# Kernel optimization log

Measured on AMD Instinct MI355X. Metric: run time of the kernel, lower is better.

The kernel has to match this reference:

```python
import jax, jax.numpy as jnp
import numpy as np

B, S, E, P, K, H = 32, 512, 1024, 256, 3, 8
KERNELS = 4  # conv repeated KERNELS times then averaged -> identical to a single conv


def setup_inputs() -> dict:
    key = jax.random.key(0)
    ks = jax.random.split(key, 8)
    sc = 0.02
    x = jax.random.normal(ks[0], (B, S, E), jnp.float32)
    # lengths must satisfy 3 <= l <= S-1 so slice [1:l+1] and conv length l-2 are valid
    seq_length = jax.random.randint(ks[1], (B,), 16, S - 1)
    proj_w = jax.random.normal(ks[2], (E, P), jnp.float32) * sc
    proj_b = jnp.zeros((P,), jnp.float32)
    conv_w = jax.random.normal(ks[3], (P, P, K), jnp.float32) * sc  # (out, in, width)
    conv_b = jnp.zeros((P,), jnp.float32)
    attn_w = jax.random.normal(ks[4], (P, H * S), jnp.float32) * sc
    attn_b = jnp.zeros((H * S,), jnp.float32)
    c1_w = jax.random.normal(ks[5], (P, P // 2), jnp.float32) * sc
    c1_b = jnp.zeros((P // 2,), jnp.float32)
    c2_w = jax.random.normal(ks[6], (P // 2, 2), jnp.float32) * sc
    c2_b = jnp.zeros((2,), jnp.float32)
    return dict(x=x, seq_length=seq_length, proj_w=proj_w, proj_b=proj_b,
                conv_w=conv_w, conv_b=conv_b, attn_w=attn_w, attn_b=attn_b,
                c1_w=c1_w, c1_b=c1_b, c2_w=c2_w, c2_b=c2_b)


def _forward(x, seq_length, proj_w, proj_b, conv_w, conv_b, attn_w, attn_b,
             c1_w, c1_b, c2_w, c2_b):
    # projection: (B,S,E) -> (B,S,P)
    proj = jnp.einsum('bse,ep->bsp', x, proj_w) + proj_b
    proj_pc = jnp.transpose(proj, (0, 2, 1))  # (B,P,S)
    # original convs each sample over slice [1:l+1]; conv is local, so conv the
    # full slice [1:] once and mask invalid tail positions per sample.
    conv = jax.lax.conv_general_dilated(
        proj_pc[:, :, 1:], conv_w, window_strides=(1,), padding='VALID',
        dimension_numbers=('NCH', 'OIH', 'NCH'))  # (B,P,S-K)
    conv = jax.nn.relu(conv + conv_b[None, :, None])
    # sum of KERNELS identical relu(conv) outputs divided by KERNELS == conv (identity)
    m = S - K  # conv output length over slice [1:]
    l = seq_length[:, None]  # (B,1)
    valid = jnp.arange(m)[None, :] < (l - (K - 1))  # output j valid iff j < l-2
    conv = jnp.where(valid[:, None, :], conv, 0.0)
    # pad: position 0 zero, conv outputs at 1..l-2, zeros after -> (B,P,S)
    rep_conv = jnp.zeros((B, P, S), conv.dtype).at[:, :, 1:1 + m].set(conv)
    rep_conv = jnp.transpose(rep_conv, (0, 2, 1))  # (B,S,P)
    # attention: logits (B,S,H*S), softmax over the FULL H*S axis (original dim=1)
    logits = jnp.einsum('bsp,pk->bsk', rep_conv, attn_w) + attn_b
    attn = jax.nn.softmax(logits, axis=-1).reshape(B, S, H, S)
    # per sample: mean over heads, sum over query rows -> weights over key pos q
    w = attn.sum(axis=(1, 2)) / H  # (B,S)
    rep_attn = jnp.einsum('bq,bqp->bp', w, rep_conv)  # (B,P)
    h = jnp.einsum('bp,ph->bh', rep_attn, c1_w) + c1_b
    h = jnp.where(h > 0, h, 0.01 * h)  # LeakyReLU(0.01)
    cls = jnp.einsum('bh,hc->bc', h, c2_w) + c2_b
    return jax.nn.softmax(cls, axis=-1)


def reference(x, seq_length, proj_w, proj_b, conv_w, conv_b, attn_w, attn_b,
              c1_w, c1_b, c2_w, c2_b):
    probs = _forward(x, seq_length, proj_w, proj_b, conv_w, conv_b,
                     attn_w, attn_b, c1_w, c1_b, c2_w, c2_b)
    return probs, jnp.argmax(probs, axis=1)
```

## Files before the change

### kernel.cpp

```cpp
#include <hip/hip_runtime.h>

#define B_ 32
#define S_ 512
#define E_ 1024
#define P_ 256
#define HH 8

typedef __attribute__((ext_vector_type(8))) short bf16x8;
typedef __attribute__((ext_vector_type(8))) unsigned short us8;
typedef __attribute__((ext_vector_type(4))) unsigned short us4;
typedef __attribute__((ext_vector_type(16))) float f32x16;

static __device__ __forceinline__ unsigned short f2bf(float f) {
  union { float f; unsigned int u; } v;
  v.f = f;
  unsigned int r = (v.u + 0x7FFFu + ((v.u >> 16) & 1u)) >> 16;
  return (unsigned short)r;
}
static __device__ __forceinline__ float bf2f(unsigned short u) {
  union { unsigned int u; float f; } v;
  v.u = ((unsigned int)u) << 16;
  return v.f;
}

__global__ __launch_bounds__(256) void k_wtT(const float* __restrict__ cw,
                                             unsigned short* __restrict__ wtT) {
  int o = blockIdx.x, k = blockIdx.y, i = threadIdx.x;
  wtT[o * 768 + k * 256 + i] = f2bf(cw[o * 768 + i * 3 + k]);
}

__global__ __launch_bounds__(256) void k_pwT(const float* __restrict__ pw,
                                             unsigned short* __restrict__ pwT) {
  __shared__ float T[32][33];
  int n0 = blockIdx.x * 32;
  int k0 = blockIdx.y * 32;
  int tx = threadIdx.x & 31, ty = threadIdx.x >> 5;
#pragma unroll
  for (int i = 0; i < 4; i++)
    T[ty + i * 8][tx] = pw[(k0 + ty + i * 8) * P_ + n0 + tx];
  __syncthreads();
#pragma unroll
  for (int i = 0; i < 4; i++)
    pwT[(size_t)(n0 + ty + i * 8) * E_ + k0 + tx] = f2bf(T[tx][ty + i * 8]);
}

__global__ __launch_bounds__(256) void k_awT(const float* __restrict__ aw,
                                             unsigned short* __restrict__ awT) {
  __shared__ float T[32][33];
  int j0 = blockIdx.x * 32;
  int k0 = blockIdx.y * 32;
  int tx = threadIdx.x & 31, ty = threadIdx.x >> 5;
#pragma unroll
  for (int i = 0; i < 4; i++)
    T[ty + i * 8][tx] = aw[(k0 + ty + i * 8) * 4096 + j0 + tx];
  __syncthreads();
#pragma unroll
  for (int i = 0; i < 4; i++)
    awT[(size_t)(j0 + ty + i * 8) * 256 + k0 + tx] = f2bf(T[tx][ty + i * 8]);
}

__global__ __launch_bounds__(256) void k_proj_mfma(const float* __restrict__ x,
                                                   const unsigned short* __restrict__ pwT,
                                                   const float* __restrict__ pb,
                                                   unsigned short* __restrict__ proj16) {
  __shared__ unsigned short As[16 * 64 * 8];
  const int m0 = blockIdx.x * 64;
  const int t = threadIdx.x;
  const int w = t >> 6, lane = t & 63, ln31 = lane & 31, kh = lane >> 5;
  const int c0 = w * 64;

  f32x16 acc00, acc01, acc10, acc11;
#pragma unroll
  for (int r = 0; r < 16; r++) { acc00[r] = 0.f; acc01[r] = 0.f; acc10[r] = 0.f; acc11[r] = 0.f; }

  const unsigned short* bp0 = pwT + (size_t)(c0 + ln31) * E_ + kh * 8;
  const unsigned short* bp1 = bp0 + (size_t)32 * E_;

  for (int kc = 0; kc < E_; kc += 128) {
#pragma unroll
    for (int i = 0; i < 8; i++) {
      int c = t + i * 256;
      int row = c >> 5, pos = c & 31;
      float4 v = *(const float4*)(x + (size_t)(m0 + row) * E_ + kc + pos * 4);
      us4 h;
      h[0] = f2bf(v.x); h[1] = f2bf(v.y); h[2] = f2bf(v.z); h[3] = f2bf(v.w);
      *(us4*)&As[((pos >> 1) * 64 + row) * 8 + (pos & 1) * 4] = h;
    }
    __syncthreads();
#pragma unroll
    for (int kk = 0; kk < 8; kk++) {
      bf16x8 a0 = *(const bf16x8*)&As[((2 * kk + kh) * 64 + ln31) * 8];
      bf16x8 a1 = *(const bf16x8*)&As[((2 * kk + kh) * 64 + 32 + ln31) * 8];
      bf16x8 b0 = *(const bf16x8*)(bp0 + kc + kk * 16);
      bf16x8 b1 = *(const bf16x8*)(bp1 + kc + kk * 16);
      acc00 = __builtin_amdgcn_mfma_f32_32x32x16_bf16(a0, b0, acc00, 0, 0, 0);
      acc01 = __builtin_amdgcn_mfma_f32_32x32x16_bf16(a0, b1, acc01, 0, 0, 0);
      acc10 = __builtin_amdgcn_mfma_f32_32x32x16_bf16(a1, b0, acc10, 0, 0, 0);
      acc11 = __builtin_amdgcn_mfma_f32_32x32x16_bf16(a1, b1, acc11, 0, 0, 0);
    }
    __syncthreads();
  }
  float pb0 = pb[c0 + ln31], pb1 = pb[c0 + 32 + ln31];
#pragma unroll
  for (int r = 0; r < 16; r++) {
    int rl = (r & 3) + 8 * (r >> 2) + 4 * kh;
    size_t g0 = (size_t)(m0 + rl) * P_;
    size_t g1 = (size_t)(m0 + 32 + rl) * P_;
    proj16[g0 + c0 + ln31]      = f2bf(acc00[r] + pb0);
    proj16[g0 + c0 + 32 + ln31] = f2bf(acc01[r] + pb1);
    proj16[g1 + c0 + ln31]      = f2bf(acc10[r] + pb0);
    proj16[g1 + c0 + 32 + ln31] = f2bf(acc11[r] + pb1);
  }
}

__global__ __launch_bounds__(256) void k_conv_mfma(const unsigned short* __restrict__ proj16,
                                                   const unsigned short* __restrict__ wtT,
                                                   const float* __restrict__ cb,
                                                   const int* __restrict__ seq,
                                                   unsigned short* __restrict__ rep16) {
  __shared__ unsigned short As[32 * 66 * 8];
  const int m0 = blockIdx.x * 64;
  const int bb = m0 >> 9, s0 = m0 & 511;
  const int t = threadIdx.x;
  const int w = t >> 6, lane = t & 63, ln31 = lane & 31, kh = lane >> 5;
  const int c0 = w * 64;

#pragma unroll
  for (int i = 0; i < 9; i++) {
    int c = t + i * 256;
    if (c < 2112) {
      int row = c >> 5, kk2 = c & 31;
      us8 v = {0, 0, 0, 0, 0, 0, 0, 0};
      if (s0 + row <= 511)
        v = *(const us8*)(proj16 + (size_t)(bb * S_ + s0 + row) * P_ + kk2 * 8);
      *(us8*)&As[(kk2 * 66 + row) * 8] = v;
    }
  }
  __syncthreads();

  f32x16 acc00, acc01, acc10, acc11;
#pragma unroll
  for (int r = 0; r < 16; r++) { acc00[r] = 0.f; acc01[r] = 0.f; acc10[r] = 0.f; acc11[r] = 0.f; }

  const unsigned short* bbase0 = wtT + (size_t)(c0 + ln31) * 768 + kh * 8;
  const unsigned short* bbase1 = bbase0 + (size_t)32 * 768;

#pragma unroll
  for (int k = 0; k < 3; k++) {
#pragma unroll
    for (int kk = 0; kk < 16; kk++) {
      bf16x8 a0 = *(const bf16x8*)&As[((2 * kk + kh) * 66 + k + ln31) * 8];
      bf16x8 a1 = *(const bf16x8*)&As[((2 * kk + kh) * 66 + k + 32 + ln31) * 8];
      bf16x8 b0 = *(const bf16x8*)(bbase0 + k * 256 + kk * 16);
      bf16x8 b1 = *(const bf16x8*)(bbase1 + k * 256 + kk * 16);
      acc00 = __builtin_amdgcn_mfma_f32_32x32x16_bf16(a0, b0, acc00, 0, 0, 0);
      acc01 = __builtin_amdgcn_mfma_f32_32x32x16_bf16(a0, b1, acc01, 0, 0, 0);
      acc10 = __builtin_amdgcn_mfma_f32_32x32x16_bf16(a1, b0, acc10, 0, 0, 0);
      acc11 = __builtin_amdgcn_mfma_f32_32x32x16_bf16(a1, b1, acc11, 0, 0, 0);
    }
  }

  int l = seq[bb];
  float cb0 = cb[c0 + ln31], cb1 = cb[c0 + 32 + ln31];
#pragma unroll
  for (int r = 0; r < 16; r++) {
    int rl = (r & 3) + 8 * (r >> 2) + 4 * kh;
    int s_a = s0 + rl, s_b = s0 + 32 + rl;
    float ma = (s_a >= 1 && s_a <= 509 && s_a < l - 1) ? 1.f : 0.f;
    float mb = (s_b >= 1 && s_b <= 509 && s_b < l - 1) ? 1.f : 0.f;
    size_t g0 = (size_t)(m0 + rl) * P_;
    size_t g1 = (size_t)(m0 + 32 + rl) * P_;
    rep16[g0 + c0 + ln31]      = f2bf(fmaxf(acc00[r] + cb0, 0.f) * ma);
    rep16[g0 + c0 + 32 + ln31] = f2bf(fmaxf(acc01[r] + cb1, 0.f) * ma);
    rep16[g1 + c0 + ln31]      = f2bf(fmaxf(acc10[r] + cb0, 0.f) * mb);
    rep16[g1 + c0 + 32 + ln31] = f2bf(fmaxf(acc11[r] + cb1, 0.f) * mb);
  }
}

__global__ __launch_bounds__(256) void k_attn_mfma(const unsigned short* __restrict__ rep16,
                                                   const unsigned short* __restrict__ awT,
                                                   const float* __restrict__ ab,
                                                   float* __restrict__ E) {
  __shared__ unsigned short As[64][264];
  const int m0 = blockIdx.x * 64;
  const int q0 = blockIdx.y * 128;
  const int t = threadIdx.x;
  const int w = t >> 6;
  const int lane = t & 63;
  const int ln31 = lane & 31;
  const int khalf = (lane >> 5) * 8;

#pragma unroll
  for (int i = 0; i < 8; i++) {
    int flat = i * 256 + t;
    int r = flat >> 5;
    int g = (flat & 31) * 8;
    us8 v = *(const us8*)(rep16 + (size_t)(m0 + r) * 256 + g);
    *(us8*)&As[r][g] = v;
  }
  __syncthreads();

  const int qcol = q0 + w * 32 + ln31;
  const unsigned short* bcol = awT + (size_t)qcol * 256 + khalf;

  float ef0[16], ef1[16];
#pragma unroll
  for (int r = 0; r < 16; r++) { ef0[r] = 0.f; ef1[r] = 0.f; }

  for (int h = 0; h < HH; h++) {
    const unsigned short* bh = bcol + (size_t)h * 512 * 256;
    f32x16 acc0, acc1;
#pragma unroll
    for (int r = 0; r < 16; r++) { acc0[r] = 0.f; acc1[r] = 0.f; }

#pragma unroll
    for (int kc = 0; kc < 256; kc += 16) {
      bf16x8 a0 = *(const bf16x8*)&As[ln31][kc + khalf];
      bf16x8 a1 = *(const bf16x8*)&As[32 + ln31][kc + khalf];
      bf16x8 b  = *(const bf16x8*)(bh + kc);
      acc0 = __builtin_amdgcn_mfma_f32_32x32x16_bf16(a0, b, acc0, 0, 0, 0);
      acc1 = __builtin_amdgcn_mfma_f32_32x32x16_bf16(a1, b, acc1, 0, 0, 0);
    }
    float bias = ab[h * 512 + qcol];
#pragma unroll
    for (int r = 0; r < 16; r++) {
      ef0[r] += __expf(acc0[r] + bias);
      ef1[r] += __expf(acc1[r] + bias);
    }
  }
  const int rbase = m0 + 4 * (lane >> 5);
#pragma unroll
  for (int r = 0; r < 16; r++) {
    int row0 = rbase + (r & 3) + 8 * (r >> 2);
    E[(size_t)row0 * 512 + qcol] = ef0[r];
    E[(size_t)(row0 + 32) * 512 + qcol] = ef1[r];
  }
}

__global__ __launch_bounds__(256) void k_z(const float* __restrict__ E,
                                           float* __restrict__ Z) {
  int row = blockIdx.x * 4 + (threadIdx.x >> 6);
  int lane = threadIdx.x & 63;
  float s = 0.f;
#pragma unroll
  for (int j = 0; j < 8; j++) s += E[(size_t)row * 512 + j * 64 + lane];
#pragma unroll
  for (int m = 32; m > 0; m >>= 1) s += __shfl_xor(s, m, 64);
  if (lane == 0) Z[row] = s;
}

__global__ __launch_bounds__(256) void k_zero(float* __restrict__ p) {
  p[blockIdx.x * 256 + threadIdx.x] = 0.f;
}

__global__ __launch_bounds__(512) void k_w(const float* __restrict__ E,
                                           const float* __restrict__ Z,
                                           float* __restrict__ wB) {
  __shared__ float rZ[64];
  int b = blockIdx.x, c = blockIdx.y, t = threadIdx.x;
  int s0 = c * 64;
  if (t < 64) rZ[t] = 1.0f / Z[b * 512 + s0 + t];
  __syncthreads();
  float acc = 0.f;
  for (int s = 0; s < 64; s++) acc += E[(size_t)(b * 512 + s0 + s) * 512 + t] * rZ[s];
  atomicAdd(&wB[b * 512 + t], acc * (1.0f / HH));
}

__global__ __launch_bounds__(256) void k_final_a(const unsigned short* __restrict__ rep16,
                                                 const float* __restrict__ wB,
                                                 float* __restrict__ repA) {
  __shared__ float wS[64];
  int b = blockIdx.x, qc = blockIdx.y, t = threadIdx.x;
  if (t < 64) wS[t] = wB[b * 512 + qc * 64 + t];
  __syncthreads();
  float acc = 0.f;
  const unsigned short* base = rep16 + (size_t)(b * 512 + qc * 64) * 256 + t;
#pragma unroll 8
  for (int q = 0; q < 64; q++) acc += wS[q] * bf2f(base[(size_t)q * 256]);
  atomicAdd(&repA[b * 256 + t], acc);
}

__global__ __launch_bounds__(128) void k_final_b(const float* __restrict__ repA,
                                                 const float* __restrict__ c1w,
                                                 const float* __restrict__ c1b,
                                                 const float* __restrict__ c2w,
                                                 const float* __restrict__ c2b,
                                                 float* __restrict__ out) {
  __shared__ float hS[128];
  __shared__ float clsS[2];
  int b = blockIdx.x, t = threadIdx.x;
  float acc = c1b[t];
  for (int p = 0; p < 256; p++) acc += repA[b * 256 + p] * c1w[p * 128 + t];
  hS[t] = acc > 0.f ? acc : 0.01f * acc;
  __syncthreads();
  if (t < 2) {
    float a2 = c2b[t];
    for (int j = 0; j < 128; j++) a2 += hS[j] * c2w[j * 2 + t];
    clsS[t] = a2;
  }
  __syncthreads();
  if (t == 0) {
    float c0 = clsS[0], c1 = clsS[1];
    float m = fmaxf(c0, c1);
    float e0 = __expf(c0 - m), e1 = __expf(c1 - m);
    float inv = 1.0f / (e0 + e1);
    float p0 = e0 * inv, p1 = e1 * inv;
    out[b * 2 + 0] = p0;
    out[b * 2 + 1] = p1;
    out[B_ * 2 + b] = (p1 > p0) ? 1.0f : 0.0f;
  }
}

extern "C" void kernel_launch(void* const* d_in, const int* in_sizes, int n_in,
                              void* d_out, int out_size, void* d_ws, size_t ws_size,
                              hipStream_t stream) {
  const float* x   = (const float*)d_in[0];
  const int*   seq = (const int*)d_in[1];
  const float* pw  = (const float*)d_in[2];
  const float* pb  = (const float*)d_in[3];
  const float* cw  = (const float*)d_in[4];
  const float* cb  = (const float*)d_in[5];
  const float* aw  = (const float*)d_in[6];
  const float* ab  = (const float*)d_in[7];
  const float* c1w = (const float*)d_in[8];
  const float* c1b = (const float*)d_in[9];
  const float* c2w = (const float*)d_in[10];
  const float* c2b = (const float*)d_in[11];
  float* out = (float*)d_out;

  char* ws = (char*)d_ws;
  unsigned short* proj16 = (unsigned short*)(ws);
  float*          E      = (float*)(ws);
  unsigned short* rep16  = (unsigned short*)(ws + (size_t)33554432);
  unsigned short* pwT    = (unsigned short*)(ws + (size_t)41943040);
  unsigned short* wtT    = (unsigned short*)(ws + (size_t)42467328);
  unsigned short* awT    = (unsigned short*)(ws + (size_t)42860544);
  float*          Z      = (float*)(ws + (size_t)44957696);
  float*          wB     = (float*)(ws + (size_t)45023232);
  float*          repA   = (float*)(ws + (size_t)45088768);

  k_wtT<<<dim3(256, 3), 256, 0, stream>>>(cw, wtT);
  k_pwT<<<dim3(8, 32), 256, 0, stream>>>(pw, pwT);
  k_awT<<<dim3(128, 8), 256, 0, stream>>>(aw, awT);
  k_proj_mfma<<<256, 256, 0, stream>>>(x, pwT, pb, proj16);
  k_conv_mfma<<<256, 256, 0, stream>>>(proj16, wtT, cb, seq, rep16);
  k_attn_mfma<<<dim3(256, 4), 256, 0, stream>>>(rep16, awT, ab, E);
  k_z<<<4096, 256, 0, stream>>>(E, Z);
  k_zero<<<96, 256, 0, stream>>>(wB);
  k_w<<<dim3(32, 8), 512, 0, stream>>>(E, Z, wB);
  k_final_a<<<dim3(32, 8), 256, 0, stream>>>(rep16, wB, repA);
  k_final_b<<<32, 128, 0, stream>>>(repA, c1w, c1b, c2w, c2b, out);
}
```

Measured before the change: 253.7 us.

## Fuse row-sum into attention kernel, store exp sums as bf16, widen N tile

The attention MFMA kernel now computes two 32-column B tiles per wave, so each block covers 256 query columns with half as many blocks. It reduces the per-row softmax denominators in-kernel with shuffles and atomics, which removes the separate k_z pass over E. E is stored as bf16 instead of fp32, halving the intermediate's write and read traffic in k_w. The cost is more accumulator registers (lower occupancy), extra atomics, and reduced precision in the stored exp sums.

```diff
diff --git a/kernel.cpp b/kernel.cpp
--- a/kernel.cpp
+++ b/kernel.cpp
@@ -57,6 +57,10 @@
 #pragma unroll
   for (int i = 0; i < 4; i++)
     awT[(size_t)(j0 + ty + i * 8) * 256 + k0 + tx] = f2bf(T[tx][ty + i * 8]);
+}
+
+__global__ __launch_bounds__(256) void k_zero(float* __restrict__ p) {
+  p[blockIdx.x * 256 + threadIdx.x] = 0.f;
 }
 
 __global__ __launch_bounds__(256) void k_proj_mfma(const float* __restrict__ x,
@@ -180,15 +184,17 @@
 __global__ __launch_bounds__(256) void k_attn_mfma(const unsigned short* __restrict__ rep16,
                                                    const unsigned short* __restrict__ awT,
                                                    const float* __restrict__ ab,
-                                                   float* __restrict__ E) {
+                                                   unsigned short* __restrict__ E16,
+                                                   float* __restrict__ Z) {
   __shared__ unsigned short As[64][264];
   const int m0 = blockIdx.x * 64;
-  const int q0 = blockIdx.y * 128;
+  const int q0 = blockIdx.y * 256;
   const int t = threadIdx.x;
   const int w = t >> 6;
   const int lane = t & 63;
   const int ln31 = lane & 31;
-  const int khalf = (lane >> 5) * 8;
+  const int kh = lane >> 5;
+  const int khalf = kh * 8;
 
 #pragma unroll
   for (int i = 0; i < 8; i++) {
@@ -200,60 +206,72 @@
   }
   __syncthreads();
 
-  const int qcol = q0 + w * 32 + ln31;
-  const unsigned short* bcol = awT + (size_t)qcol * 256 + khalf;
-
-  float ef0[16], ef1[16];
-#pragma unroll
-  for (int r = 0; r < 16; r++) { ef0[r] = 0.f; ef1[r] = 0.f; }
+  const int qb = q0 + w * 64;
+  const int qc0 = qb + ln31;
+  const int qc1 = qb + 32 + ln31;
+
+  float ef00[16], ef01[16], ef10[16], ef11[16];
+#pragma unroll
+  for (int r = 0; r < 16; r++) { ef00[r] = 0.f; ef01[r] = 0.f; ef10[r] = 0.f; ef11[r] = 0.f; }
 
   for (int h = 0; h < HH; h++) {
-    const unsigned short* bh = bcol + (size_t)h * 512 * 256;
-    f32x16 acc0, acc1;
-#pragma unroll
-    for (int r = 0; r < 16; r++) { acc0[r] = 0.f; acc1[r] = 0.f; }
+    const unsigned short* b0p = awT + (size_t)(h * 512 + qc0) * 256 + khalf;
+    const unsigned short* b1p = awT + (size_t)(h * 512 + qc1) * 256 + khalf;
+    f32x16 acc00, acc01, acc10, acc11;
+#pragma unroll
+    for (int r = 0; r < 16; r++) { acc00[r] = 0.f; acc01[r] = 0.f; acc10[r] = 0.f; acc11[r] = 0.f; }
 
 #pragma unroll
     for (int kc = 0; kc < 256; kc += 16) {
       bf16x8 a0 = *(const bf16x8*)&As[ln31][kc + khalf];
       bf16x8 a1 = *(const bf16x8*)&As[32 + ln31][kc + khalf];
-      bf16x8 b  = *(const bf16x8*)(bh + kc);
-      acc0 = __builtin_amdgcn_mfma_f32_32x32x16_bf16(a0, b, acc0, 0, 0, 0);
-      acc1 = __builtin_amdgcn_mfma_f32_32x32x16_bf16(a1, b, acc1, 0, 0, 0);
-    }
-    float bias = ab[h * 512 + qcol];
+      bf16x8 b0 = *(const bf16x8*)(b0p + kc);
+      bf16x8 b1 = *(const bf16x8*)(b1p + kc);
+      acc00 = __builtin_amdgcn_mfma_f32_32x32x16_bf16(a0, b0, acc00, 0, 0, 0);
+      acc01 = __builtin_amdgcn_mfma_f32_32x32x16_bf16(a0, b1, acc01, 0, 0, 0);
+      acc10 = __builtin_amdgcn_mfma_f32_32x32x16_bf16(a1, b0, acc10, 0, 0, 0);
+      acc11 = __builtin_amdgcn_mfma_f32_32x32x16_bf16(a1, b1, acc11, 0, 0, 0);
+    }
+    float bias0 = ab[h * 512 + qc0];
+    float bias1 = ab[h * 512 + qc1];
 #pragma unroll
     for (int r = 0; r < 16; r++) {
-      ef0[r] += __expf(acc0[r] + bias);
-      ef1[r] += __expf(acc1[r] + bias);
-    }
-  }
-  const int rbase = m0 + 4 * (lane >> 5);
+      ef00[r] += __expf(acc00[r] + bias0);
+      ef01[r] += __expf(acc01[r] + bias1);
+      ef10[r] += __expf(acc10[r] + bias0);
+      ef11[r] += __expf(acc11[r] + bias1);
+    }
+  }
+
 #pragma unroll
   for (int r = 0; r < 16; r++) {
-    int row0 = rbase + (r & 3) + 8 * (r >> 2);
-    E[(size_t)row0 * 512 + qcol] = ef0[r];
-    E[(size_t)(row0 + 32) * 512 + qcol] = ef1[r];
-  }
-}
-
-__global__ __launch_bounds__(256) void k_z(const float* __restrict__ E,
-                                           float* __restrict__ Z) {
-  int row = blockIdx.x * 4 + (threadIdx.x >> 6);
-  int lane = threadIdx.x & 63;
-  float s = 0.f;
-#pragma unroll
-  for (int j = 0; j < 8; j++) s += E[(size_t)row * 512 + j * 64 + lane];
-#pragma unroll
-  for (int m = 32; m > 0; m >>= 1) s += __shfl_xor(s, m, 64);
-  if (lane == 0) Z[row] = s;
-}
-
-__global__ __launch_bounds__(256) void k_zero(float* __restrict__ p) {
-  p[blockIdx.x * 256 + threadIdx.x] = 0.f;
-}
-
-__global__ __launch_bounds__(512) void k_w(const float* __restrict__ E,
+    int rl = (r & 3) + 8 * (r >> 2) + 4 * kh;
+    size_t row0 = (size_t)(m0 + rl) * 512;
+    size_t row1 = (size_t)(m0 + 32 + rl) * 512;
+    E16[row0 + qc0] = f2bf(ef00[r]);
+    E16[row0 + qc1] = f2bf(ef01[r]);
+    E16[row1 + qc0] = f2bf(ef10[r]);
+    E16[row1 + qc1] = f2bf(ef11[r]);
+  }
+
+#pragma unroll
+  for (int r = 0; r < 16; r++) {
+    float z0 = ef00[r] + ef01[r];
+    float z1 = ef10[r] + ef11[r];
+#pragma unroll
+    for (int st = 16; st >= 1; st >>= 1) {
+      z0 += __shfl_xor(z0, st, 64);
+      z1 += __shfl_xor(z1, st, 64);
+    }
+    if (ln31 == 0) {
+      int rl = (r & 3) + 8 * (r >> 2) + 4 * kh;
+      atomicAdd(&Z[m0 + rl], z0);
+      atomicAdd(&Z[m0 + 32 + rl], z1);
+    }
+  }
+}
+
+__global__ __launch_bounds__(512) void k_w(const unsigned short* __restrict__ E16,
                                            const float* __restrict__ Z,
                                            float* __restrict__ wB) {
   __shared__ float rZ[64];
@@ -262,7 +280,9 @@
   if (t < 64) rZ[t] = 1.0f / Z[b * 512 + s0 + t];
   __syncthreads();
   float acc = 0.f;
-  for (int s = 0; s < 64; s++) acc += E[(size_t)(b * 512 + s0 + s) * 512 + t] * rZ[s];
+#pragma unroll 8
+  for (int s = 0; s < 64; s++)
+    acc += bf2f(E16[(size_t)(b * 512 + s0 + s) * 512 + t]) * rZ[s];
   atomicAdd(&wB[b * 512 + t], acc * (1.0f / HH));
 }
 
@@ -330,24 +350,23 @@
 
   char* ws = (char*)d_ws;
   unsigned short* proj16 = (unsigned short*)(ws);
-  float*          E      = (float*)(ws);
-  unsigned short* rep16  = (unsigned short*)(ws + (size_t)33554432);
-  unsigned short* pwT    = (unsigned short*)(ws + (size_t)41943040);
-  unsigned short* wtT    = (unsigned short*)(ws + (size_t)42467328);
-  unsigned short* awT    = (unsigned short*)(ws + (size_t)42860544);
-  float*          Z      = (float*)(ws + (size_t)44957696);
-  float*          wB     = (float*)(ws + (size_t)45023232);
-  float*          repA   = (float*)(ws + (size_t)45088768);
-
+  unsigned short* E16    = (unsigned short*)(ws);
+  unsigned short* rep16  = (unsigned short*)(ws + (size_t)16777216);
+  unsigned short* pwT    = (unsigned short*)(ws + (size_t)25165824);
+  unsigned short* wtT    = (unsigned short*)(ws + (size_t)25690112);
+  unsigned short* awT    = (unsigned short*)(ws + (size_t)26083328);
+  float*          Z      = (float*)(ws + (size_t)28180480);
+  float*          wB     = (float*)(ws + (size_t)28246016);
+  float*          repA   = (float*)(ws + (size_t)28311552);
+
+  k_zero<<<160, 256, 0, stream>>>(Z);
   k_wtT<<<dim3(256, 3), 256, 0, stream>>>(cw, wtT);
   k_pwT<<<dim3(8, 32), 256, 0, stream>>>(pw, pwT);
   k_awT<<<dim3(128, 8), 256, 0, stream>>>(aw, awT);
   k_proj_mfma<<<256, 256, 0, stream>>>(x, pwT, pb, proj16);
   k_conv_mfma<<<256, 256, 0, stream>>>(proj16, wtT, cb, seq, rep16);
-  k_attn_mfma<<<dim3(256, 4), 256, 0, stream>>>(rep16, awT, ab, E);
-  k_z<<<4096, 256, 0, stream>>>(E, Z);
-  k_zero<<<96, 256, 0, stream>>>(wB);
-  k_w<<<dim3(32, 8), 512, 0, stream>>>(E, Z, wB);
+  k_attn_mfma<<<dim3(256, 2), 256, 0, stream>>>(rep16, awT, ab, E16, Z);
+  k_w<<<dim3(32, 8), 512, 0, stream>>>(E16, Z, wB);
   k_final_a<<<dim3(32, 8), 256, 0, stream>>>(rep16, wB, repA);
   k_final_b<<<32, 128, 0, stream>>>(repA, c1w, c1b, c2w, c2b, out);
 }
```

Result: slower. 276.8 us (+9.1%).
